# Performance work log

Hardware: AMD Instinct MI355X
Metric: run time of the kernel (lower is better)

## Reference

```python
import jax, jax.numpy as jnp
import numpy as np
from jax import lax

FEAT = 16; STRIDE = 16; IMG = 256; K = 30; POOL = 7
NMS_TH = 0.85; TEMP = 0.07; B = 32; CLIP_DIM = 1024; PROJ = 256; NA = 9

def _anchors():
    scales = [8.0, 16.0, 32.0]; ratios = [0.5, 1.0, 2.0]
    A = []
    for i in range(FEAT):
        for j in range(FEAT):
            xc = (j + 0.5) * STRIDE; yc = (i + 0.5) * STRIDE
            for s in scales:
                for r in ratios:
                    w = s * r ** 0.5; h = s / r ** 0.5
                    A.append([xc - w / 2, yc - h / 2, xc + w / 2, yc + h / 2])
    return jnp.asarray(np.array(A, dtype=np.float32))  # [2304,4]

def _decode(reg, anchors):
    wh = anchors[:, 2:] - anchors[:, :2]; ctr = anchors[:, :2] + 0.5 * wh
    cx = reg[..., 0] * wh[:, 0] + ctr[:, 0]; cy = reg[..., 1] * wh[:, 1] + ctr[:, 1]
    pw = jnp.exp(reg[..., 2]) * wh[:, 0]; ph = jnp.exp(reg[..., 3]) * wh[:, 1]
    b = jnp.stack([cx - 0.5 * pw, cy - 0.5 * ph, cx + 0.5 * pw, cy + 0.5 * ph], -1)
    b = jnp.clip(b, 0.0, 256.0)
    x1, y1, x2, y2 = b[..., 0], b[..., 1], b[..., 2], b[..., 3]
    x2 = jnp.where(x2 - x1 < 1, x1 + 1, x2)
    y2 = jnp.where(y2 - y1 < 1, y1 + 1, y2)
    return jnp.stack([x1, y1, x2, y2], -1)

def _nms_keep(b):  # [K,4], already sorted by score desc
    x1, y1, x2, y2 = b[:, 0], b[:, 1], b[:, 2], b[:, 3]
    area = (x2 - x1) * (y2 - y1)
    iw = jnp.clip(jnp.minimum(x2[:, None], x2[None]) - jnp.maximum(x1[:, None], x1[None]), 0)
    ih = jnp.clip(jnp.minimum(y2[:, None], y2[None]) - jnp.maximum(y1[:, None], y1[None]), 0)
    inter = iw * ih
    iou = inter / (area[:, None] + area[None] - inter)
    idx = jnp.arange(K)
    def body(i, keep):
        supp = (idx > i) & (iou[i] > NMS_TH) & keep[i]
        return keep & ~supp
    return lax.fori_loop(0, K, body, jnp.ones(K, bool))

def _roi_align_mean(feats, bidx, rois):
    # roi_align(output 7x7, spatial_scale=1/16, sampling_ratio=1) then mean over bins
    N = rois.shape[0]; _, C, H, W = feats.shape
    sc = 1.0 / STRIDE
    x1, y1 = rois[:, 0] * sc, rois[:, 1] * sc
    rw = jnp.maximum(rois[:, 2] * sc - x1, 1.0); rh = jnp.maximum(rois[:, 3] * sc - y1, 1.0)
    g = jnp.arange(POOL, dtype=feats.dtype) + 0.5
    xs = x1[:, None] + g[None] * (rw / POOL)[:, None]  # [N,7]
    ys = y1[:, None] + g[None] * (rh / POOL)[:, None]
    X = jnp.broadcast_to(xs[:, None, :], (N, POOL, POOL))
    Y = jnp.broadcast_to(ys[:, :, None], (N, POOL, POOL))
    ok = (Y > -1) & (Y < H) & (X > -1) & (X < W)
    Xc = jnp.clip(X, 0, W - 1); Yc = jnp.clip(Y, 0, H - 1)
    x0 = jnp.floor(Xc).astype(jnp.int32); y0 = jnp.floor(Yc).astype(jnp.int32)
    x1i = jnp.minimum(x0 + 1, W - 1); y1i = jnp.minimum(y0 + 1, H - 1)
    lx = Xc - x0; ly = Yc - y0; hx = 1 - lx; hy = 1 - ly
    bN = bidx[:, None, None]
    f00 = feats[bN, :, y0, x0]; f01 = feats[bN, :, y0, x1i]  # [N,7,7,C]
    f10 = feats[bN, :, y1i, x0]; f11 = feats[bN, :, y1i, x1i]
    v = ((hy * hx)[..., None] * f00 + (hy * lx)[..., None] * f01
         + (ly * hx)[..., None] * f10 + (ly * lx)[..., None] * f11)
    v = v * ok[..., None]
    return v.mean(axis=(1, 2))  # [N,C]

def _roi_labels(gt_masks, bidx, rois):
    g = gt_masks[:, 0]  # [B,256,256]
    I = jnp.pad(jnp.cumsum(jnp.cumsum(g, 1), 2), ((0, 0), (1, 0), (1, 0)))  # integral image
    c = jnp.clip(rois.astype(jnp.int32), 0, IMG)
    x1, y1, x2, y2 = c[:, 0], c[:, 1], c[:, 2], c[:, 3]
    s = I[bidx, y2, x2] - I[bidx, y1, x2] - I[bidx, y2, x1] + I[bidx, y1, x1]
    cnt = (y2 - y1) * (x2 - x1)
    return jnp.where(cnt > 0, s / jnp.maximum(cnt, 1) > 0.5, False)

def _supcon(proj, labels, valid):
    nf = proj / jnp.clip(jnp.linalg.norm(proj, axis=1, keepdims=True), 1e-12)
    sim = (nf @ nf.T) / TEMP
    N = proj.shape[0]
    nd = ~jnp.eye(N, dtype=bool)
    vv = valid[:, None] & valid[None]
    pos = (labels[:, None] == labels[None]) & nd & vv
    vmask = nd & vv
    es = jnp.exp(sim)
    ratio = (es * pos).sum(1) / ((es * vmask).sum(1) + 1e-12)
    l = -jnp.log(ratio + 1e-12)
    active = valid & (pos.sum(1) > 0)
    cnt = active.sum()
    return jnp.where(cnt > 0, (l * active).sum() / jnp.maximum(cnt, 1), 0.0)

def _forward(clip_features, gt_masks, conv_w, conv_b, cls_w, cls_b, reg_w, reg_b,
             proj_w1, proj_b1, proj_w2, proj_b2):
    Bn = clip_features.shape[1]
    spatial = jnp.transpose(clip_features[1:], (1, 2, 0)).reshape(Bn, CLIP_DIM, FEAT, FEAT)
    x = jax.nn.relu(lax.conv_general_dilated(
        spatial, conv_w, (1, 1), 'SAME',
        dimension_numbers=('NCHW', 'OIHW', 'NCHW')) + conv_b[None, :, None, None])
    cls = jnp.einsum('bchw,ac->bahw', x, cls_w) + cls_b[None, :, None, None]
    reg = jnp.einsum('bchw,ac->bahw', x, reg_w) + reg_b[None, :, None, None]
    reg_p = reg.reshape(Bn, NA, 4, FEAT, FEAT).transpose(0, 3, 4, 1, 2).reshape(Bn, -1, 4)
    cls_p = cls.transpose(0, 2, 3, 1).reshape(Bn, -1)
    boxes = _decode(reg_p, _anchors())  # [B,2304,4]
    scores = jax.nn.sigmoid(cls_p)
    _, top_i = lax.top_k(scores, K)
    top_boxes = jnp.take_along_axis(boxes, top_i[..., None], axis=1)  # [B,K,4]
    keep = jax.vmap(_nms_keep)(top_boxes)  # [B,K]
    rois = lax.stop_gradient(top_boxes.reshape(-1, 4))  # torch roi_align/labels don't backprop thru roi coords
    valid = keep.reshape(-1)
    bidx = jnp.repeat(jnp.arange(Bn), K)
    pooled = _roi_align_mean(spatial, bidx, rois)  # [N,1024]
    h = jax.nn.relu(pooled @ proj_w1.T + proj_b1)
    proj = h @ proj_w2.T + proj_b2  # [N,256]
    labels = _roi_labels(gt_masks, bidx, rois)
    return _supcon(proj, labels, valid)

def setup_inputs() -> dict:
    key = jax.random.key(0)
    ks = jax.random.split(key, 8)
    s = 0.02
    return {
        'clip_features': jax.random.normal(ks[0], (257, B, CLIP_DIM), jnp.float32),
        'gt_masks': (jax.random.uniform(ks[1], (B, 1, IMG, IMG)) > 0.5).astype(jnp.float32),
        'conv_w': jax.random.normal(ks[2], (512, CLIP_DIM, 3, 3)) * s,
        'conv_b': jnp.zeros((512,)),
        'cls_w': jax.random.normal(ks[3], (NA, 512)) * s,
        'cls_b': jnp.zeros((NA,)),
        'reg_w': jax.random.normal(ks[4], (NA * 4, 512)) * s,
        'reg_b': jnp.zeros((NA * 4,)),
        'proj_w1': jax.random.normal(ks[5], (PROJ, CLIP_DIM)) * s,
        'proj_b1': jnp.zeros((PROJ,)),
        'proj_w2': jax.random.normal(ks[6], (PROJ, PROJ)) * s,
        'proj_b2': jnp.zeros((PROJ,)),
    }

def reference(clip_features, gt_masks, conv_w, conv_b, cls_w, cls_b, reg_w, reg_b,
              proj_w1, proj_b1, proj_w2, proj_b2):
    return _forward(clip_features, gt_masks, conv_w, conv_b, cls_w, cls_b, reg_w, reg_b,
                    proj_w1, proj_b1, proj_w2, proj_b2)
```

## Files before the change

kernel.cpp:

```cpp
#include <hip/hip_runtime.h>
#include <hip/hip_bf16.h>
#include <math.h>

typedef unsigned short u16;
typedef unsigned int u32;
typedef _Float16 f16;
typedef _Float16 f16x8 __attribute__((ext_vector_type(8)));
typedef float f32x4 __attribute__((ext_vector_type(4)));

#define BATCH 32
#define CIN   1024
#define COUT  512
#define NPOS  8192
#define K9    9216
#define KHALF 4608
#define TOPK  30
#define NROI  960
#define POOLN 7
#define IMG   256
#define SJT   15
#define HB_POS 32

#define O_XP0  0ull
#define O_XP1  4194304ull
#define O_CH   8388608ull
#define O_CL   12582912ull
#define O_WH   16777216ull
#define O_WL   19136512ull
#define O_Z    21495808ull
#define O_HW   21496064ull
#define O_SC   21519104ull
#define O_RG   21592832ull
#define O_ROI  21887744ull
#define O_VAL  21891584ull
#define O_LAB  21892544ull
#define O_W1T  21893504ull
#define O_W2T  22155648ull
#define WS_FLOATS 22221184ull
#define O_PO   0ull
#define O_NF   1474560ull
#define O_PS   1720320ull

__device__ __forceinline__ void gl_lds16(const void* g, void* l) {
    __builtin_amdgcn_global_load_lds(
        (const __attribute__((address_space(1))) u32*)g,
        (__attribute__((address_space(3))) u32*)l,
        16, 0, 0);
}

__device__ inline void split16(float x, u16& h, u16& l) {
    f16 hv = (f16)x;
    f16 lv = (f16)(x - (float)hv);
    h = *(u16*)&hv;
    l = *(u16*)&lv;
}

#define NB_CLIP 8192
#define NB_W    2048
#define NB_Z    1
#define NB_HW   90
#define NB_W1T  1024
#define NB_W2T  256
__global__ __launch_bounds__(256)
void convert_all(const float* __restrict__ clip, const float* __restrict__ conv_w,
                 const float* __restrict__ cls_w, const float* __restrict__ reg_w,
                 const float* __restrict__ w1, const float* __restrict__ w2,
                 u16* __restrict__ CH, u16* __restrict__ CL,
                 u16* __restrict__ WH, u16* __restrict__ WL,
                 u16* __restrict__ Z, float* __restrict__ HW,
                 float* __restrict__ w1T, float* __restrict__ w2T) {
    __shared__ float wsh[2304];
    int bid = blockIdx.x, t = threadIdx.x;
    if (bid < NB_CLIP) {
        int tid = bid * 256 + t;
        int c4  = (tid & 255) * 4;
        int pos = (tid >> 8) & 255;
        int b   = tid >> 16;
        float4 v = *(const float4*)(clip + ((size_t)(1 + pos) * 32 + b) * 1024 + c4);
        float xs[4] = {v.x, v.y, v.z, v.w};
        ushort4 hh, ll;
        u16* hp = (u16*)&hh; u16* lp = (u16*)&ll;
#pragma unroll
        for (int q = 0; q < 4; ++q) split16(xs[q], hp[q], lp[q]);
        size_t o = ((size_t)(b * 256 + pos)) * 1024 + c4;
        *(ushort4*)(CH + o) = hh;
        *(ushort4*)(CL + o) = ll;
    } else if (bid < NB_CLIP + NB_W) {
        int bid2 = bid - NB_CLIP;
        int o = bid2 >> 2, cblk = bid2 & 3;
        const float* src = conv_w + (size_t)o * K9 + cblk * 2304;
        for (int i = t; i < 2304; i += 256) wsh[i] = src[i];
        __syncthreads();
#pragma unroll
        for (int p = 0; p < 9; ++p) {
            float x = wsh[t * 9 + p];
            u16 h, l;
            split16(x, h, l);
            size_t o2 = (size_t)o * K9 + p * 1024 + cblk * 256 + t;
            WH[o2] = h; WL[o2] = l;
        }
    } else if (bid < NB_CLIP + NB_W + NB_Z) {
        Z[t] = 0; Z[256 + t] = 0;
    } else if (bid < NB_CLIP + NB_W + NB_Z + NB_HW) {
        int tid2 = (bid - NB_CLIP - NB_W - NB_Z) * 256 + t;
        if (tid2 < 45 * 512) {
            int a = tid2 >> 9, c = tid2 & 511;
            HW[tid2] = (a < 9) ? cls_w[a * 512 + c] : reg_w[(a - 9) * 512 + c];
        }
    } else if (bid < NB_CLIP + NB_W + NB_Z + NB_HW + NB_W1T) {
        int tid2 = (bid - NB_CLIP - NB_W - NB_Z - NB_HW) * 256 + t;
        int o = tid2 >> 10, c = tid2 & 1023;
        w1T[c * 256 + o] = w1[(size_t)o * 1024 + c];
    } else {
        int tid2 = (bid - NB_CLIP - NB_W - NB_Z - NB_HW - NB_W1T) * 256 + t;
        int o = tid2 >> 8, c = tid2 & 255;
        w2T[c * 256 + o] = w2[(size_t)o * 256 + c];
    }
}

__global__ __launch_bounds__(256, 2)
void conv_mfma(const u16* __restrict__ CH, const u16* __restrict__ CL,
               const u16* __restrict__ WH, const u16* __restrict__ WL,
               const u16* __restrict__ ZS,
               float* __restrict__ XP0, float* __restrict__ XP1) {
    __shared__ __align__(16) u16 Ah[8192];
    __shared__ __align__(16) u16 Al[8192];
    __shared__ __align__(16) u16 Bh[8192];
    __shared__ __align__(16) u16 Bl[8192];

    const int t = threadIdx.x;
    const int gid = blockIdx.x;
    const int nb = gid >> 7;
    const int g  = gid & 127;
    const int mb = g >> 1;
    const int ks = g & 1;
    const int ksOff = ks * KHALF;
    float* __restrict__ XP = ks ? XP1 : XP0;

    const int wave = t >> 6, lane = t & 63;

    int qA[2], siA[2], sjA[2], bA[2];
    const u16* srcBh[2];
    const u16* srcBl[2];
#pragma unroll
    for (int j = 0; j < 2; ++j) {
        int r = wave * 32 + j * 16 + (lane >> 2);
        int s = lane & 3;
        int q = s ^ ((r >> 1) & 3);
        qA[j] = q;
        int m = mb * 128 + r;
        bA[j] = m >> 8;
        int ij = m & 255;
        siA[j] = ij >> 4; sjA[j] = ij & 15;
        int o = nb * 128 + r;
        srcBh[j] = WH + (size_t)o * K9 + q * 8;
        srcBl[j] = WL + (size_t)o * K9 + q * 8;
    }

    const int wm = wave >> 1, wn = wave & 1;
    const int l16 = lane & 15, quad = lane >> 4;
    int offA[4], offB[4];
#pragma unroll
    for (int q = 0; q < 4; ++q) {
        int ar = wm * 64 + q * 16 + l16;
        offA[q] = ar * 32 + ((quad ^ ((ar >> 1) & 3)) << 3);
        int br = wn * 64 + q * 16 + l16;
        offB[q] = br * 32 + ((quad ^ ((br >> 1) & 3)) << 3);
    }

    f32x4 acc[4][4];
#pragma unroll
    for (int r = 0; r < 4; ++r)
#pragma unroll
        for (int c = 0; c < 4; ++c) acc[r][c] = (f32x4){0.f, 0.f, 0.f, 0.f};

    auto issue = [&](int it, int buf) {
        const int kg = ksOff + it * 32;
        const int p = kg >> 10;
        const int cb = kg & 1023;
        const int di = p / 3, dj = p - di * 3;
        const int base = buf << 12;
#pragma unroll
        for (int j = 0; j < 2; ++j) {
            int ii = siA[j] + di - 1, jj = sjA[j] + dj - 1;
            bool ok = ((unsigned)ii < 16u) && ((unsigned)jj < 16u);
            size_t aoff = ok ? ((((size_t)bA[j] << 8) + (size_t)(ii * 16 + jj)) << 10) + cb + qA[j] * 8
                             : 0;
            const u16* gah = ok ? CH + aoff : ZS;
            const u16* gal = ok ? CL + aoff : ZS;
            int lb = base + wave * 1024 + j * 512;
            gl_lds16(gah,           &Ah[lb]);
            gl_lds16(gal,           &Al[lb]);
            gl_lds16(srcBh[j] + kg, &Bh[lb]);
            gl_lds16(srcBl[j] + kg, &Bl[lb]);
        }
    };

    issue(0, 0);
    for (int it = 0; it < 144; ++it) {
        const int cur = it & 1;
        __syncthreads();
        if (it + 1 < 144) issue(it + 1, cur ^ 1);

        const int fb = cur << 12;
        f16x8 fah[4], fal[4], fbh[4], fbl[4];
#pragma unroll
        for (int x = 0; x < 4; ++x) {
            fah[x] = *(const f16x8*)&Ah[fb + offA[x]];
            fal[x] = *(const f16x8*)&Al[fb + offA[x]];
            fbh[x] = *(const f16x8*)&Bh[fb + offB[x]];
            fbl[x] = *(const f16x8*)&Bl[fb + offB[x]];
        }
#pragma unroll
        for (int tm = 0; tm < 4; ++tm)
#pragma unroll
            for (int tn = 0; tn < 4; ++tn) {
                acc[tm][tn] = __builtin_amdgcn_mfma_f32_16x16x32_f16(fal[tm], fbh[tn], acc[tm][tn], 0, 0, 0);
                acc[tm][tn] = __builtin_amdgcn_mfma_f32_16x16x32_f16(fah[tm], fbl[tn], acc[tm][tn], 0, 0, 0);
                acc[tm][tn] = __builtin_amdgcn_mfma_f32_16x16x32_f16(fah[tm], fbh[tn], acc[tm][tn], 0, 0, 0);
            }
    }

#pragma unroll
    for (int tm = 0; tm < 4; ++tm) {
        int mbase = mb * 128 + wm * 64 + tm * 16 + quad * 4;
#pragma unroll
        for (int tn = 0; tn < 4; ++tn) {
            int o = nb * 128 + wn * 64 + tn * 16 + l16;
#pragma unroll
            for (int r = 0; r < 4; ++r)
                XP[(size_t)(mbase + r) * COUT + o] = acc[tm][tn][r];
        }
    }
}

__global__ __launch_bounds__(256)
void heads_kernel(const float* __restrict__ XP0, const float* __restrict__ XP1,
                  const float* __restrict__ conv_b, const float* __restrict__ HWT,
                  const float* __restrict__ cls_b, const float* __restrict__ reg_b,
                  float* __restrict__ scores, float* __restrict__ regs) {
    __shared__ __align__(16) float Xs[HB_POS * 512];
    __shared__ __align__(16) float Ws[45 * 512];
    int t = threadIdx.x;
    int mm0 = blockIdx.x * HB_POS;

    for (int idx = t; idx < HB_POS * 128; idx += 256) {
        int p = idx >> 7, cq = idx & 127;
        int mm = mm0 + p;
        float4 a = *(const float4*)(XP0 + (size_t)mm * COUT + cq * 4);
        float4 b = *(const float4*)(XP1 + (size_t)mm * COUT + cq * 4);
        float4 cv = *(const float4*)(conv_b + cq * 4);
        float4 r;
        r.x = fmaxf(a.x + b.x + cv.x, 0.f);
        r.y = fmaxf(a.y + b.y + cv.y, 0.f);
        r.z = fmaxf(a.z + b.z + cv.z, 0.f);
        r.w = fmaxf(a.w + b.w + cv.w, 0.f);
        int byte_off = ((p << 11) + (cq << 4)) ^ ((p & 7) << 4);
        *(float4*)((char*)Xs + byte_off) = r;
    }
    for (int idx = t; idx < 5760; idx += 256)
        ((float4*)Ws)[idx] = ((const float4*)HWT)[idx];
    __syncthreads();

    int w = t >> 6, lane = t & 63;
    int p = lane & 31, half = lane >> 5;
    const char* xrow = (const char*)Xs + (p << 11) + (half << 10);
    const int swz = (p & 7) << 4;
    int a0 = w * 12;
    const float* wrow[12];
#pragma unroll
    for (int k = 0; k < 12; ++k) {
        int ak = a0 + k; if (ak > 44) ak = 44;
        wrow[k] = Ws + ak * 512 + half * 256;
    }

    float acc[12];
#pragma unroll
    for (int k = 0; k < 12; ++k) acc[k] = 0.f;
    for (int cq = 0; cq < 64; ++cq) {
        float4 x4 = *(const float4*)(xrow + ((cq << 4) ^ swz));
#pragma unroll
        for (int k = 0; k < 12; ++k) {
            float4 w4 = *(const float4*)(wrow[k] + cq * 4);
            acc[k] = fmaf(x4.x, w4.x, acc[k]);
            acc[k] = fmaf(x4.y, w4.y, acc[k]);
            acc[k] = fmaf(x4.z, w4.z, acc[k]);
            acc[k] = fmaf(x4.w, w4.w, acc[k]);
        }
    }
#pragma unroll
    for (int k = 0; k < 12; ++k) acc[k] += __shfl_xor(acc[k], 32);

    if (half == 0) {
        int mm = mm0 + p;
        int b = mm >> 8, cell = mm & 255;
#pragma unroll
        for (int k = 0; k < 12; ++k) {
            int a = a0 + k;
            if (a < 45) {
                if (a < 9) {
                    float v = acc[k] + cls_b[a];
                    scores[(size_t)b * 2304 + cell * 9 + a] = 1.f / (1.f + expf(-v));
                } else {
                    int ch = a - 9;
                    float v = acc[k] + reg_b[ch];
                    regs[((size_t)b * 2304 + cell * 9 + (ch >> 2)) * 4 + (ch & 3)] = v;
                }
            }
        }
    }
}

__global__ __launch_bounds__(256)
void topk_nms(const float* __restrict__ scores, const float* __restrict__ regs,
              float* __restrict__ rois, float* __restrict__ valid) {
    __shared__ float sc[2304];
    __shared__ float wv[4];
    __shared__ int   wi[4];
    __shared__ int   sel[TOPK];
    __shared__ float bx[TOPK][4];
    __shared__ float iou[TOPK * TOPK];
    __shared__ float keepsh[TOPK];
    int b = blockIdx.x, t = threadIdx.x;
    for (int q = t; q < 2304; q += 256) sc[q] = scores[(size_t)b * 2304 + q];
    __syncthreads();

    for (int k = 0; k < TOPK; ++k) {
        float bv = -1e30f; int bi = 1 << 30;
#pragma unroll
        for (int q = 0; q < 9; ++q) {
            int idx = t * 9 + q;
            float v = sc[idx];
            if (v > bv || (v == bv && idx < bi)) { bv = v; bi = idx; }
        }
        for (int off = 32; off; off >>= 1) {
            float ov = __shfl_down(bv, off);
            int   oi = __shfl_down(bi, off);
            if (ov > bv || (ov == bv && oi < bi)) { bv = ov; bi = oi; }
        }
        int lane = t & 63, w = t >> 6;
        if (lane == 0) { wv[w] = bv; wi[w] = bi; }
        __syncthreads();
        if (t == 0) {
            float fv = wv[0]; int fi = wi[0];
            for (int q = 1; q < 4; ++q)
                if (wv[q] > fv || (wv[q] == fv && wi[q] < fi)) { fv = wv[q]; fi = wi[q]; }
            sel[k] = fi;
            sc[fi] = -1e38f;
        }
        __syncthreads();
    }

    if (t < TOPK) {
        int n = sel[t];
        int cell = n / 9, a = n % 9;
        int ci = cell >> 4, cj = cell & 15;
        int siid = a / 3, riid = a % 3;
        const double scl[3] = {8.0, 16.0, 32.0};
        const double rat[3] = {0.5, 1.0, 2.0};
        double s = scl[siid], r = rat[riid];
        double wD = s * sqrt(r), hD = s / sqrt(r);
        double xc = (cj + 0.5) * 16.0, yc = (ci + 0.5) * 16.0;
        float ax1 = (float)(xc - wD / 2), ay1 = (float)(yc - hD / 2);
        float ax2 = (float)(xc + wD / 2), ay2 = (float)(yc + hD / 2);
        float aw = ax2 - ax1, ah = ay2 - ay1;
        float ctrx = ax1 + 0.5f * aw, ctry = ay1 + 0.5f * ah;
        const float* rg = regs + ((size_t)b * 2304 + n) * 4;
        float cx = rg[0] * aw + ctrx;
        float cy = rg[1] * ah + ctry;
        float pw = expf(rg[2]) * aw;
        float ph = expf(rg[3]) * ah;
        float x1 = cx - 0.5f * pw, y1 = cy - 0.5f * ph;
        float x2 = cx + 0.5f * pw, y2 = cy + 0.5f * ph;
        x1 = fminf(fmaxf(x1, 0.f), 256.f);
        y1 = fminf(fmaxf(y1, 0.f), 256.f);
        x2 = fminf(fmaxf(x2, 0.f), 256.f);
        y2 = fminf(fmaxf(y2, 0.f), 256.f);
        if (x2 - x1 < 1.f) x2 = x1 + 1.f;
        if (y2 - y1 < 1.f) y2 = y1 + 1.f;
        bx[t][0] = x1; bx[t][1] = y1; bx[t][2] = x2; bx[t][3] = y2;
        keepsh[t] = 1.f;
    }
    __syncthreads();
    if (t < TOPK * TOPK) {
        int ii = t / TOPK, jj = t % TOPK;
        float xi1 = bx[ii][0], yi1 = bx[ii][1], xi2 = bx[ii][2], yi2 = bx[ii][3];
        float xj1 = bx[jj][0], yj1 = bx[jj][1], xj2 = bx[jj][2], yj2 = bx[jj][3];
        float ai = (xi2 - xi1) * (yi2 - yi1), aj = (xj2 - xj1) * (yj2 - yj1);
        float iw = fmaxf(fminf(xi2, xj2) - fmaxf(xi1, xj1), 0.f);
        float ih = fmaxf(fminf(yi2, yj2) - fmaxf(yi1, yj1), 0.f);
        float inter = iw * ih;
        iou[t] = inter / (ai + aj - inter);
    }
    __syncthreads();
    for (int iK = 0; iK < TOPK - 1; ++iK) {
        if (t > iK && t < TOPK) {
            if (keepsh[iK] > 0.5f && iou[iK * TOPK + t] > 0.85f) keepsh[t] = 0.f;
        }
        __syncthreads();
    }
    if (t < TOPK) {
        int rr = b * TOPK + t;
        rois[rr * 4 + 0] = bx[t][0]; rois[rr * 4 + 1] = bx[t][1];
        rois[rr * 4 + 2] = bx[t][2]; rois[rr * 4 + 3] = bx[t][3];
        valid[rr] = keepsh[t];
    }
}

__global__ __launch_bounds__(256)
void align_img(const float* __restrict__ clip, const float* __restrict__ rois,
               float* __restrict__ pooled) {
    __shared__ float slice[16384];
    int bid = blockIdx.x;
    int b = bid >> 4, cg = bid & 15;
    int t = threadIdx.x;
    for (int idx = t; idx < 16384; idx += 256) {
        int p = idx >> 6, c = idx & 63;
        slice[idx] = clip[(size_t)(1 + p) * 32768 + (size_t)b * 1024 + cg * 64 + c];
    }
    __syncthreads();
    int wv = t >> 6;
    int ch = t & 63;
    for (int rp = 0; rp < 8; ++rp) {
        int rl = rp * 4 + wv;
        if (rl >= TOPK) continue;
        int r = b * TOPK + rl;
        float rx1 = rois[r * 4 + 0] * 0.0625f, ry1 = rois[r * 4 + 1] * 0.0625f;
        float rw = fmaxf(rois[r * 4 + 2] * 0.0625f - rx1, 1.f);
        float rh = fmaxf(rois[r * 4 + 3] * 0.0625f - ry1, 1.f);
        float sx = rw / (float)POOLN, sy = rh / (float)POOLN;
        float acc = 0.f;
        for (int py = 0; py < POOLN; ++py) {
            float Y = ry1 + ((float)py + 0.5f) * sy;
            for (int px = 0; px < POOLN; ++px) {
                float Xx = rx1 + ((float)px + 0.5f) * sx;
                bool ok = (Y > -1.f) && (Y < 16.f) && (Xx > -1.f) && (Xx < 16.f);
                if (!ok) continue;
                float Xc = fminf(fmaxf(Xx, 0.f), 15.f);
                float Yc = fminf(fmaxf(Y, 0.f), 15.f);
                int x0 = (int)floorf(Xc), y0 = (int)floorf(Yc);
                int x1i = min(x0 + 1, 15), y1i = min(y0 + 1, 15);
                float lx = Xc - (float)x0, ly = Yc - (float)y0;
                float hx = 1.f - lx, hy = 1.f - ly;
                float w00 = hy * hx, w01 = hy * lx, w10 = ly * hx, w11 = ly * lx;
                float f00 = slice[(y0 * 16 + x0) * 64 + ch];
                float f01 = slice[(y0 * 16 + x1i) * 64 + ch];
                float f10 = slice[(y1i * 16 + x0) * 64 + ch];
                float f11 = slice[(y1i * 16 + x1i) * 64 + ch];
                acc += w00 * f00 + w01 * f01 + w10 * f10 + w11 * f11;
            }
        }
        pooled[(size_t)r * 1024 + cg * 64 + ch] = acc / 49.f;
    }
}

__global__ __launch_bounds__(256)
void labels_k(const float* __restrict__ gt, const float* __restrict__ rois,
              float* __restrict__ labels) {
    __shared__ float red[4];
    int r = blockIdx.x, t = threadIdx.x;
    int b = r / TOPK;
    int x1 = min(max((int)rois[r * 4 + 0], 0), 256);
    int y1 = min(max((int)rois[r * 4 + 1], 0), 256);
    int x2 = min(max((int)rois[r * 4 + 2], 0), 256);
    int y2 = min(max((int)rois[r * 4 + 3], 0), 256);
    int cnt = (x2 - x1) * (y2 - y1);
    float s = 0.f;
    if (cnt > 0) {
        const float* g = gt + (size_t)b * (IMG * IMG);
        for (int yy = y1; yy < y2; ++yy) {
            const float* row = g + yy * IMG;
            for (int xx = x1 + t; xx < x2; xx += 256) s += row[xx];
        }
    }
    for (int off = 32; off; off >>= 1) s += __shfl_down(s, off);
    if ((t & 63) == 0) red[t >> 6] = s;
    __syncthreads();
    if (t == 0) {
        float tot = red[0] + red[1] + red[2] + red[3];
        labels[r] = (cnt > 0 && 2.f * tot > (float)cnt) ? 1.f : 0.f;
    }
}

__global__ __launch_bounds__(256)
void fc_norm(const float* __restrict__ pooled, const float* __restrict__ w1T,
             const float* __restrict__ b1, const float* __restrict__ w2T,
             const float* __restrict__ b2, float* __restrict__ nf) {
    __shared__ float rows[4][1024];
    __shared__ float hsh[4][256];
    __shared__ float red[4];
    int r0 = blockIdx.x * 4, t = threadIdx.x;
    for (int q = 0; q < 4; ++q)
        for (int c = t; c < 1024; c += 256)
            rows[q][c] = pooled[(size_t)(r0 + q) * 1024 + c];
    __syncthreads();
    {
        float bv = b1[t];
        float acc[4] = {bv, bv, bv, bv};
        for (int c = 0; c < 1024; ++c) {
            float wv = w1T[c * 256 + t];
#pragma unroll
            for (int q = 0; q < 4; ++q) acc[q] = fmaf(rows[q][c], wv, acc[q]);
        }
#pragma unroll
        for (int q = 0; q < 4; ++q) hsh[q][t] = fmaxf(acc[q], 0.f);
    }
    __syncthreads();
    float pr[4];
    {
        float bv = b2[t];
        float acc[4] = {bv, bv, bv, bv};
        for (int c = 0; c < 256; ++c) {
            float wv = w2T[c * 256 + t];
#pragma unroll
            for (int q = 0; q < 4; ++q) acc[q] = fmaf(hsh[q][c], wv, acc[q]);
        }
#pragma unroll
        for (int q = 0; q < 4; ++q) pr[q] = acc[q];
    }
    for (int q = 0; q < 4; ++q) {
        float v = pr[q];
        float ss = v * v;
        for (int off = 32; off; off >>= 1) ss += __shfl_down(ss, off);
        if ((t & 63) == 0) red[t >> 6] = ss;
        __syncthreads();
        float tot = red[0] + red[1] + red[2] + red[3];
        float denom = fmaxf(sqrtf(tot), 1e-12f);
        nf[(size_t)(r0 + q) * 256 + t] = v / denom;
        __syncthreads();
    }
}

__global__ __launch_bounds__(256)
void supcon_tile(const float* __restrict__ nf, const float* __restrict__ labels,
                 const float* __restrict__ valid, float* __restrict__ PS) {
    __shared__ __align__(16) float nfT[64 * 256];
    __shared__ __align__(16) float myl[32 * 256];
    __shared__ float labj[64], valj[64];
    int bid = blockIdx.x;
    int it = bid / SJT, jt = bid - it * SJT;
    int i0 = it * 32, j0 = jt * 64;
    int t = threadIdx.x;

    for (int idx = t; idx < 64 * 256; idx += 256) {
        int j = idx >> 8, c = idx & 255;
        float v = nf[(size_t)(j0 + j) * 256 + c];
        int byte_off = ((j << 10) + (c << 2)) ^ ((j & 7) << 4);
        *(float*)((char*)nfT + byte_off) = v;
    }
    for (int idx = t; idx < 32 * 256; idx += 256)
        myl[idx] = nf[(size_t)i0 * 256 + idx];
    if (t < 64) { labj[t] = labels[j0 + t]; valj[t] = valid[j0 + t]; }
    __syncthreads();

    int w = t >> 6, lane = t & 63;
    const char* jrow = (const char*)nfT + (lane << 10);
    const int sw = (lane & 7) << 4;
    const float* my0 = &myl[(w * 8) * 256];

    float d[8];
#pragma unroll
    for (int q = 0; q < 8; ++q) d[q] = 0.f;
    for (int c = 0; c < 256; c += 4) {
        float4 b4 = *(const float4*)(jrow + ((c << 2) ^ sw));
#pragma unroll
        for (int q = 0; q < 8; ++q) {
            float4 a4 = *(const float4*)(my0 + q * 256 + c);
            d[q] = fmaf(a4.x, b4.x, d[q]);
            d[q] = fmaf(a4.y, b4.y, d[q]);
            d[q] = fmaf(a4.z, b4.z, d[q]);
            d[q] = fmaf(a4.w, b4.w, d[q]);
        }
    }

    int jg = j0 + lane;
    float vj = valj[lane], lj = labj[lane];
#pragma unroll
    for (int q = 0; q < 8; ++q) {
        int ig = i0 + w * 8 + q;
        float vi = valid[ig];
        float li = labels[ig];
        bool vmask = (vi > 0.5f) && (vj > 0.5f) && (jg != ig);
        float e  = vmask ? expf(d[q] / 0.07f) : 0.f;
        bool pos = vmask && (lj == li);
        float ep  = pos ? e : 0.f;
        float npv = pos ? 1.f : 0.f;
        float sa = e, sp = ep, sn = npv;
#pragma unroll
        for (int off = 32; off; off >>= 1) {
            sa += __shfl_xor(sa, off);
            sp += __shfl_xor(sp, off);
            sn += __shfl_xor(sn, off);
        }
        if (lane == 0) {
            size_t o = ((size_t)ig * SJT + jt) * 3;
            PS[o + 0] = sa;
            PS[o + 1] = sp;
            PS[o + 2] = sn;
        }
    }
}

__global__ __launch_bounds__(256)
void final_reduce2(const float* __restrict__ PS, const float* __restrict__ valid,
                   float* __restrict__ out) {
    __shared__ float rl[4], ra[4];
    int t = threadIdx.x;
    float sl = 0.f, sc = 0.f;
    for (int i = t; i < NROI; i += 256) {
        float sa = 0.f, sp = 0.f, np = 0.f;
        for (int jt = 0; jt < SJT; ++jt) {
            size_t o = ((size_t)i * SJT + jt) * 3;
            sa += PS[o + 0];
            sp += PS[o + 1];
            np += PS[o + 2];
        }
        bool active = (valid[i] > 0.5f) && (np > 0.5f);
        float ratio = sp / (sa + 1e-12f);
        float l = -logf(ratio + 1e-12f);
        sl += active ? l : 0.f;
        sc += active ? 1.f : 0.f;
    }
    for (int off = 32; off; off >>= 1) { sl += __shfl_down(sl, off); sc += __shfl_down(sc, off); }
    if ((t & 63) == 0) { rl[t >> 6] = sl; ra[t >> 6] = sc; }
    __syncthreads();
    if (t == 0) {
        float L = rl[0] + rl[1] + rl[2] + rl[3];
        float A = ra[0] + ra[1] + ra[2] + ra[3];
        out[0] = (A > 0.f) ? (L / fmaxf(A, 1.f)) : 0.f;
    }
}

extern "C" void kernel_launch(void* const* d_in, const int* in_sizes, int n_in,
                              void* d_out, int out_size, void* d_ws, size_t ws_size,
                              hipStream_t stream) {
    const float* clip   = (const float*)d_in[0];
    const float* gt     = (const float*)d_in[1];
    const float* conv_w = (const float*)d_in[2];
    const float* conv_b = (const float*)d_in[3];
    const float* cls_w  = (const float*)d_in[4];
    const float* cls_b  = (const float*)d_in[5];
    const float* reg_w  = (const float*)d_in[6];
    const float* reg_b  = (const float*)d_in[7];
    const float* w1     = (const float*)d_in[8];
    const float* b1     = (const float*)d_in[9];
    const float* w2     = (const float*)d_in[10];
    const float* b2     = (const float*)d_in[11];

    if (ws_size < WS_FLOATS * sizeof(float)) return;

    float* ws  = (float*)d_ws;
    float* XP0 = ws + O_XP0;
    float* XP1 = ws + O_XP1;
    u16*   CH  = (u16*)(ws + O_CH);
    u16*   CL  = (u16*)(ws + O_CL);
    u16*   WHp = (u16*)(ws + O_WH);
    u16*   WLp = (u16*)(ws + O_WL);
    u16*   ZS  = (u16*)(ws + O_Z);
    float* HW  = ws + O_HW;
    float* SC  = ws + O_SC;
    float* RG  = ws + O_RG;
    float* ROI = ws + O_ROI;
    float* VAL = ws + O_VAL;
    float* LAB = ws + O_LAB;
    float* W1T = ws + O_W1T;
    float* W2T = ws + O_W2T;
    float* PO  = ws + O_PO;
    float* NF  = ws + O_NF;
    float* PS  = ws + O_PS;

    convert_all<<<NB_CLIP + NB_W + NB_Z + NB_HW + NB_W1T + NB_W2T, 256, 0, stream>>>(
        clip, conv_w, cls_w, reg_w, w1, w2, CH, CL, WHp, WLp, ZS, HW, W1T, W2T);
    conv_mfma<<<512, 256, 0, stream>>>(CH, CL, WHp, WLp, ZS, XP0, XP1);
    heads_kernel<<<NPOS / HB_POS, 256, 0, stream>>>(XP0, XP1, conv_b, HW, cls_b, reg_b, SC, RG);
    topk_nms<<<BATCH, 256, 0, stream>>>(SC, RG, ROI, VAL);
    align_img<<<512, 256, 0, stream>>>(clip, ROI, PO);
    labels_k<<<NROI, 256, 0, stream>>>(gt, ROI, LAB);
    fc_norm<<<NROI / 4, 256, 0, stream>>>(PO, W1T, b1, W2T, b2, NF);
    supcon_tile<<<30 * SJT, 256, 0, stream>>>(NF, LAB, VAL, PS);
    final_reduce2<<<1, 256, 0, stream>>>(PS, VAL, (float*)d_out);
}
```

Measured before the change: 602.9 us.

## Register-resident top-k, merge ROI align and label kernels, vectorize fc_norm

The top-k selection now keeps each thread's nine scores in registers and uses double-buffered warp results, which removes one barrier per iteration. The ROI align and label kernels are merged into one launch with heterogeneous blocks, saving a launch and letting the two kinds of work overlap. fc_norm now uses float4 shared-memory reads with four weights loaded per step. The main cost is still the conv GEMM, so these small-kernel tweaks touch only a minor share of the time.

```diff
diff --git a/kernel.cpp b/kernel.cpp
--- a/kernel.cpp
+++ b/kernel.cpp
@@ -314,42 +314,43 @@
 __global__ __launch_bounds__(256)
 void topk_nms(const float* __restrict__ scores, const float* __restrict__ regs,
               float* __restrict__ rois, float* __restrict__ valid) {
-    __shared__ float sc[2304];
-    __shared__ float wv[4];
-    __shared__ int   wi[4];
+    __shared__ float wv[2][4];
+    __shared__ int   wi[2][4];
     __shared__ int   sel[TOPK];
     __shared__ float bx[TOPK][4];
     __shared__ float iou[TOPK * TOPK];
     __shared__ float keepsh[TOPK];
     int b = blockIdx.x, t = threadIdx.x;
-    for (int q = t; q < 2304; q += 256) sc[q] = scores[(size_t)b * 2304 + q];
-    __syncthreads();
+    int lane = t & 63, w = t >> 6;
+    float v[9];
+#pragma unroll
+    for (int q = 0; q < 9; ++q) v[q] = scores[(size_t)b * 2304 + t * 9 + q];
 
     for (int k = 0; k < TOPK; ++k) {
+        int kb = k & 1;
         float bv = -1e30f; int bi = 1 << 30;
 #pragma unroll
         for (int q = 0; q < 9; ++q) {
             int idx = t * 9 + q;
-            float v = sc[idx];
-            if (v > bv || (v == bv && idx < bi)) { bv = v; bi = idx; }
+            if (v[q] > bv || (v[q] == bv && idx < bi)) { bv = v[q]; bi = idx; }
         }
         for (int off = 32; off; off >>= 1) {
             float ov = __shfl_down(bv, off);
             int   oi = __shfl_down(bi, off);
             if (ov > bv || (ov == bv && oi < bi)) { bv = ov; bi = oi; }
         }
-        int lane = t & 63, w = t >> 6;
-        if (lane == 0) { wv[w] = bv; wi[w] = bi; }
-        __syncthreads();
-        if (t == 0) {
-            float fv = wv[0]; int fi = wi[0];
-            for (int q = 1; q < 4; ++q)
-                if (wv[q] > fv || (wv[q] == fv && wi[q] < fi)) { fv = wv[q]; fi = wi[q]; }
-            sel[k] = fi;
-            sc[fi] = -1e38f;
-        }
-        __syncthreads();
-    }
+        if (lane == 0) { wv[kb][w] = bv; wi[kb][w] = bi; }
+        __syncthreads();
+        float fv = wv[kb][0]; int fi = wi[kb][0];
+#pragma unroll
+        for (int q2 = 1; q2 < 4; ++q2)
+            if (wv[kb][q2] > fv || (wv[kb][q2] == fv && wi[kb][q2] < fi)) { fv = wv[kb][q2]; fi = wi[kb][q2]; }
+        if (t == 0) sel[k] = fi;
+#pragma unroll
+        for (int q = 0; q < 9; ++q)
+            if (t * 9 + q == fi) v[q] = -1e38f;
+    }
+    __syncthreads();
 
     if (t < TOPK) {
         int n = sel[t];
@@ -408,77 +409,75 @@
 }
 
 __global__ __launch_bounds__(256)
-void align_img(const float* __restrict__ clip, const float* __restrict__ rois,
-               float* __restrict__ pooled) {
+void roi_post(const float* __restrict__ clip, const float* __restrict__ rois,
+              float* __restrict__ pooled,
+              const float* __restrict__ gt, float* __restrict__ labels) {
     __shared__ float slice[16384];
     int bid = blockIdx.x;
-    int b = bid >> 4, cg = bid & 15;
     int t = threadIdx.x;
-    for (int idx = t; idx < 16384; idx += 256) {
-        int p = idx >> 6, c = idx & 63;
-        slice[idx] = clip[(size_t)(1 + p) * 32768 + (size_t)b * 1024 + cg * 64 + c];
-    }
-    __syncthreads();
-    int wv = t >> 6;
-    int ch = t & 63;
-    for (int rp = 0; rp < 8; ++rp) {
-        int rl = rp * 4 + wv;
-        if (rl >= TOPK) continue;
-        int r = b * TOPK + rl;
-        float rx1 = rois[r * 4 + 0] * 0.0625f, ry1 = rois[r * 4 + 1] * 0.0625f;
-        float rw = fmaxf(rois[r * 4 + 2] * 0.0625f - rx1, 1.f);
-        float rh = fmaxf(rois[r * 4 + 3] * 0.0625f - ry1, 1.f);
-        float sx = rw / (float)POOLN, sy = rh / (float)POOLN;
-        float acc = 0.f;
-        for (int py = 0; py < POOLN; ++py) {
-            float Y = ry1 + ((float)py + 0.5f) * sy;
-            for (int px = 0; px < POOLN; ++px) {
-                float Xx = rx1 + ((float)px + 0.5f) * sx;
-                bool ok = (Y > -1.f) && (Y < 16.f) && (Xx > -1.f) && (Xx < 16.f);
-                if (!ok) continue;
-                float Xc = fminf(fmaxf(Xx, 0.f), 15.f);
-                float Yc = fminf(fmaxf(Y, 0.f), 15.f);
-                int x0 = (int)floorf(Xc), y0 = (int)floorf(Yc);
-                int x1i = min(x0 + 1, 15), y1i = min(y0 + 1, 15);
-                float lx = Xc - (float)x0, ly = Yc - (float)y0;
-                float hx = 1.f - lx, hy = 1.f - ly;
-                float w00 = hy * hx, w01 = hy * lx, w10 = ly * hx, w11 = ly * lx;
-                float f00 = slice[(y0 * 16 + x0) * 64 + ch];
-                float f01 = slice[(y0 * 16 + x1i) * 64 + ch];
-                float f10 = slice[(y1i * 16 + x0) * 64 + ch];
-                float f11 = slice[(y1i * 16 + x1i) * 64 + ch];
-                acc += w00 * f00 + w01 * f01 + w10 * f10 + w11 * f11;
+    if (bid < 512) {
+        int b = bid >> 4, cg = bid & 15;
+        for (int idx = t; idx < 16384; idx += 256) {
+            int p = idx >> 6, c = idx & 63;
+            slice[idx] = clip[(size_t)(1 + p) * 32768 + (size_t)b * 1024 + cg * 64 + c];
+        }
+        __syncthreads();
+        int wv = t >> 6;
+        int ch = t & 63;
+        for (int rp = 0; rp < 8; ++rp) {
+            int rl = rp * 4 + wv;
+            if (rl >= TOPK) continue;
+            int r = b * TOPK + rl;
+            float rx1 = rois[r * 4 + 0] * 0.0625f, ry1 = rois[r * 4 + 1] * 0.0625f;
+            float rw = fmaxf(rois[r * 4 + 2] * 0.0625f - rx1, 1.f);
+            float rh = fmaxf(rois[r * 4 + 3] * 0.0625f - ry1, 1.f);
+            float sx = rw / (float)POOLN, sy = rh / (float)POOLN;
+            float acc = 0.f;
+            for (int py = 0; py < POOLN; ++py) {
+                float Y = ry1 + ((float)py + 0.5f) * sy;
+                for (int px = 0; px < POOLN; ++px) {
+                    float Xx = rx1 + ((float)px + 0.5f) * sx;
+                    bool ok = (Y > -1.f) && (Y < 16.f) && (Xx > -1.f) && (Xx < 16.f);
+                    if (!ok) continue;
+                    float Xc = fminf(fmaxf(Xx, 0.f), 15.f);
+                    float Yc = fminf(fmaxf(Y, 0.f), 15.f);
+                    int x0 = (int)floorf(Xc), y0 = (int)floorf(Yc);
+                    int x1i = min(x0 + 1, 15), y1i = min(y0 + 1, 15);
+                    float lx = Xc - (float)x0, ly = Yc - (float)y0;
+                    float hx = 1.f - lx, hy = 1.f - ly;
+                    float w00 = hy * hx, w01 = hy * lx, w10 = ly * hx, w11 = ly * lx;
+                    float f00 = slice[(y0 * 16 + x0) * 64 + ch];
+                    float f01 = slice[(y0 * 16 + x1i) * 64 + ch];
+                    float f10 = slice[(y1i * 16 + x0) * 64 + ch];
+                    float f11 = slice[(y1i * 16 + x1i) * 64 + ch];
+                    acc += w00 * f00 + w01 * f01 + w10 * f10 + w11 * f11;
+                }
             }
-        }
-        pooled[(size_t)r * 1024 + cg * 64 + ch] = acc / 49.f;
-    }
-}
-
-__global__ __launch_bounds__(256)
-void labels_k(const float* __restrict__ gt, const float* __restrict__ rois,
-              float* __restrict__ labels) {
-    __shared__ float red[4];
-    int r = blockIdx.x, t = threadIdx.x;
-    int b = r / TOPK;
-    int x1 = min(max((int)rois[r * 4 + 0], 0), 256);
-    int y1 = min(max((int)rois[r * 4 + 1], 0), 256);
-    int x2 = min(max((int)rois[r * 4 + 2], 0), 256);
-    int y2 = min(max((int)rois[r * 4 + 3], 0), 256);
-    int cnt = (x2 - x1) * (y2 - y1);
-    float s = 0.f;
-    if (cnt > 0) {
-        const float* g = gt + (size_t)b * (IMG * IMG);
-        for (int yy = y1; yy < y2; ++yy) {
-            const float* row = g + yy * IMG;
-            for (int xx = x1 + t; xx < x2; xx += 256) s += row[xx];
-        }
-    }
-    for (int off = 32; off; off >>= 1) s += __shfl_down(s, off);
-    if ((t & 63) == 0) red[t >> 6] = s;
-    __syncthreads();
-    if (t == 0) {
-        float tot = red[0] + red[1] + red[2] + red[3];
-        labels[r] = (cnt > 0 && 2.f * tot > (float)cnt) ? 1.f : 0.f;
+            pooled[(size_t)r * 1024 + cg * 64 + ch] = acc / 49.f;
+        }
+    } else {
+        int r = bid - 512;
+        int b = r / TOPK;
+        int x1 = min(max((int)rois[r * 4 + 0], 0), 256);
+        int y1 = min(max((int)rois[r * 4 + 1], 0), 256);
+        int x2 = min(max((int)rois[r * 4 + 2], 0), 256);
+        int y2 = min(max((int)rois[r * 4 + 3], 0), 256);
+        int cnt = (x2 - x1) * (y2 - y1);
+        float s = 0.f;
+        if (cnt > 0) {
+            const float* g = gt + (size_t)b * (IMG * IMG);
+            for (int yy = y1; yy < y2; ++yy) {
+                const float* row = g + yy * IMG;
+                for (int xx = x1 + t; xx < x2; xx += 256) s += row[xx];
+            }
+        }
+        for (int off = 32; off; off >>= 1) s += __shfl_down(s, off);
+        if ((t & 63) == 0) slice[t >> 6] = s;
+        __syncthreads();
+        if (t == 0) {
+            float tot = slice[0] + slice[1] + slice[2] + slice[3];
+            labels[r] = (cnt > 0 && 2.f * tot > (float)cnt) ? 1.f : 0.f;
+        }
     }
 }
 
@@ -486,21 +485,30 @@
 void fc_norm(const float* __restrict__ pooled, const float* __restrict__ w1T,
              const float* __restrict__ b1, const float* __restrict__ w2T,
              const float* __restrict__ b2, float* __restrict__ nf) {
-    __shared__ float rows[4][1024];
-    __shared__ float hsh[4][256];
+    __shared__ __align__(16) float rows[4][1024];
+    __shared__ __align__(16) float hsh[4][256];
     __shared__ float red[4];
     int r0 = blockIdx.x * 4, t = threadIdx.x;
+#pragma unroll
     for (int q = 0; q < 4; ++q)
-        for (int c = t; c < 1024; c += 256)
-            rows[q][c] = pooled[(size_t)(r0 + q) * 1024 + c];
+        *(float4*)&rows[q][t * 4] = *(const float4*)(pooled + (size_t)(r0 + q) * 1024 + t * 4);
     __syncthreads();
     {
         float bv = b1[t];
         float acc[4] = {bv, bv, bv, bv};
-        for (int c = 0; c < 1024; ++c) {
-            float wv = w1T[c * 256 + t];
-#pragma unroll
-            for (int q = 0; q < 4; ++q) acc[q] = fmaf(rows[q][c], wv, acc[q]);
+        for (int c = 0; c < 1024; c += 4) {
+            float w0 = w1T[(c + 0) * 256 + t];
+            float w1v = w1T[(c + 1) * 256 + t];
+            float w2v = w1T[(c + 2) * 256 + t];
+            float w3v = w1T[(c + 3) * 256 + t];
+#pragma unroll
+            for (int q = 0; q < 4; ++q) {
+                float4 x4 = *(const float4*)&rows[q][c];
+                acc[q] = fmaf(x4.x, w0, acc[q]);
+                acc[q] = fmaf(x4.y, w1v, acc[q]);
+                acc[q] = fmaf(x4.z, w2v, acc[q]);
+                acc[q] = fmaf(x4.w, w3v, acc[q]);
+            }
         }
 #pragma unroll
         for (int q = 0; q < 4; ++q) hsh[q][t] = fmaxf(acc[q], 0.f);
@@ -510,10 +518,19 @@
     {
         float bv = b2[t];
         float acc[4] = {bv, bv, bv, bv};
-        for (int c = 0; c < 256; ++c) {
-            float wv = w2T[c * 256 + t];
-#pragma unroll
-            for (int q = 0; q < 4; ++q) acc[q] = fmaf(hsh[q][c], wv, acc[q]);
+        for (int c = 0; c < 256; c += 4) {
+            float w0 = w2T[(c + 0) * 256 + t];
+            float w1v = w2T[(c + 1) * 256 + t];
+            float w2v = w2T[(c + 2) * 256 + t];
+            float w3v = w2T[(c + 3) * 256 + t];
+#pragma unroll
+            for (int q = 0; q < 4; ++q) {
+                float4 x4 = *(const float4*)&hsh[q][c];
+                acc[q] = fmaf(x4.x, w0, acc[q]);
+                acc[q] = fmaf(x4.y, w1v, acc[q]);
+                acc[q] = fmaf(x4.z, w2v, acc[q]);
+                acc[q] = fmaf(x4.w, w3v, acc[q]);
+            }
         }
 #pragma unroll
         for (int q = 0; q < 4; ++q) pr[q] = acc[q];
@@ -674,8 +691,7 @@
     conv_mfma<<<512, 256, 0, stream>>>(CH, CL, WHp, WLp, ZS, XP0, XP1);
     heads_kernel<<<NPOS / HB_POS, 256, 0, stream>>>(XP0, XP1, conv_b, HW, cls_b, reg_b, SC, RG);
     topk_nms<<<BATCH, 256, 0, stream>>>(SC, RG, ROI, VAL);
-    align_img<<<512, 256, 0, stream>>>(clip, ROI, PO);
-    labels_k<<<NROI, 256, 0, stream>>>(gt, ROI, LAB);
+    roi_post<<<512 + NROI, 256, 0, stream>>>(clip, ROI, PO, gt, LAB);
     fc_norm<<<NROI / 4, 256, 0, stream>>>(PO, W1T, b1, W2T, b2, NF);
     supcon_tile<<<30 * SJT, 256, 0, stream>>>(NF, LAB, VAL, PS);
     final_reduce2<<<1, 256, 0, stream>>>(PS, VAL, (float*)d_out);
```

Measured after the change: 561.7 us. -6.8%, faster.
